# Kernel optimization log

Hardware: AMD Instinct MI355X
Metric: run time of the kernel (lower is better)

The kernel has to match this reference:

```python
import jax, jax.numpy as jnp
import numpy as np

TEMPERATURE_F = 0.5  # temperature_f from __init__


def setup_inputs() -> dict:
    key = jax.random.key(0)
    k1, k2 = jax.random.split(key)
    B, D = 4096, 512
    h_i = jax.random.normal(k1, (B, D), dtype=jnp.float32)
    h_j = jax.random.normal(k2, (B, D), dtype=jnp.float32)
    return {"h_i": h_i, "h_j": h_j}


def reference(h_i, h_j) -> jnp.ndarray:
    # NT-Xent loss (forward_private). N = 2*batch_size.
    B = h_i.shape[0]
    N = 2 * B
    h = jnp.concatenate([h_i, h_j], axis=0)          # [N, D]
    sim = (h @ h.T) / TEMPERATURE_F                   # [N, N]

    # Positive pairs: sim[i, i+B] and sim[i+B, i]
    sim_i_j = jnp.diagonal(sim, offset=B)             # [B]
    sim_j_i = jnp.diagonal(sim, offset=-B)            # [B]
    pos = jnp.concatenate([sim_i_j, sim_j_i], axis=0)  # [N]

    # Original builds logits = [pos | negatives] where negatives are the row of
    # sim with the diagonal and the positive entry removed, and labels are 0.
    # Cross-entropy per row = -pos_i + logsumexp(pos_i, negatives_i)
    #                       = -pos_i + logsumexp over row i of sim excluding the
    #                         diagonal (the positive entry equals pos_i, so the
    #                         set of logsumexp'd values is identical).
    neg_inf = jnp.finfo(sim.dtype).min
    diag = jnp.eye(N, dtype=bool)
    sim_masked = jnp.where(diag, neg_inf, sim)        # exclude self-similarity
    lse = jax.nn.logsumexp(sim_masked, axis=1)        # [N]

    loss = jnp.sum(lse - pos) / N                     # CE sum reduction, / N
    return loss
```

## Files before the change

kernel.cpp:

```cpp
#include <hip/hip_runtime.h>
#include <hip/hip_bf16.h>
#include <float.h>

#define BN_ 4096
#define DD  512
#define NN  8192
#define SCALE 2.0f

typedef unsigned short u16;
typedef __attribute__((ext_vector_type(8))) short short8;
typedef __attribute__((ext_vector_type(4))) float floatx4;

struct alignas(8) U16x4 { u16 x, y, z, w; };

__device__ __forceinline__ u16 f2bf(float f) {
    union { float f; unsigned u; } c; c.f = f;
    unsigned u = c.u;
    unsigned r = (u + 0x7fffu + ((u >> 16) & 1u)) >> 16;
    return (u16)r;
}

__device__ __forceinline__ void async_copy16(const u16* g, u16* l) {
    __builtin_amdgcn_global_load_lds(
        (const __attribute__((address_space(1))) void*)g,
        (__attribute__((address_space(3))) void*)l, 16, 0, 0);
}

__global__ __launch_bounds__(256) void convert_pos_kernel(const float* __restrict__ hi,
                                                          const float* __restrict__ hj,
                                                          u16* __restrict__ H,
                                                          float* __restrict__ out) {
    __shared__ float red[4];
    int t = blockIdx.x * 256 + threadIdx.x;
    int e = t * 4;
    const int BD = BN_ * DD;
    float4 a = *(const float4*)(hi + e);
    float4 b = *(const float4*)(hj + e);
    U16x4 oa, ob;
    oa.x = f2bf(a.x); oa.y = f2bf(a.y); oa.z = f2bf(a.z); oa.w = f2bf(a.w);
    ob.x = f2bf(b.x); ob.y = f2bf(b.y); ob.z = f2bf(b.z); ob.w = f2bf(b.w);
    *(U16x4*)(H + e) = oa;
    *(U16x4*)(H + BD + e) = ob;
    float dot = a.x * b.x + a.y * b.y + a.z * b.z + a.w * b.w;
#pragma unroll
    for (int msk = 1; msk < 64; msk <<= 1) dot += __shfl_xor(dot, msk);
    int lane = threadIdx.x & 63, wid = threadIdx.x >> 6;
    if (lane == 0) red[wid] = dot;
    __syncthreads();
    if (threadIdx.x == 0) {
        float s = red[0] + red[1] + red[2] + red[3];
        atomicAdd(out, s * (-4.0f / (float)NN));
    }
}

__global__ __launch_bounds__(256, 3) void gram_kernel(const u16* __restrict__ H,
                                                      float* __restrict__ Mpart,
                                                      float* __restrict__ Spart) {
    __shared__ u16 As[128 * 64];
    __shared__ u16 Bs[128 * 64];
    __shared__ float Rm[2][128], Rs[2][128];
    __shared__ float Cm[2][128], Cs[2][128];

    const int tid  = threadIdx.x;
    const int lane = tid & 63;
    const int wid  = tid >> 6;
    const int quad = lane >> 4;
    const int ln15 = lane & 15;
    const int wr = wid >> 1, wc = wid & 1;

    int t = blockIdx.x;
    int bi = (int)((sqrtf(8.0f * (float)t + 1.0f) - 1.0f) * 0.5f);
    while ((bi + 1) * (bi + 2) / 2 <= t) bi++;
    while (bi * (bi + 1) / 2 > t) bi--;
    const int bj = t - bi * (bi + 1) / 2;
    const bool diag = (bi == bj);
    const int biBase = bi * 128, bjBase = bj * 128;

    const u16* srcA[4];
    int ldsOff[4];
#pragma unroll
    for (int j = 0; j < 4; j++) {
        int c   = j * 256 + tid;
        int row = c >> 3;
        int kc  = (c & 7) ^ (row & 7);
        srcA[j]   = H + (size_t)(biBase + row) * DD + kc * 8;
        ldsOff[j] = c * 8;
    }
    const ptrdiff_t dB = (ptrdiff_t)(bjBase - biBase) * DD;

    floatx4 acc[4][4];
#pragma unroll
    for (int i = 0; i < 4; i++)
#pragma unroll
        for (int j = 0; j < 4; j++) acc[i][j] = (floatx4)0.0f;

    for (int k0 = 0; k0 < DD; k0 += 64) {
#pragma unroll
        for (int j = 0; j < 4; j++) async_copy16(srcA[j] + k0,      &As[ldsOff[j]]);
#pragma unroll
        for (int j = 0; j < 4; j++) async_copy16(srcA[j] + dB + k0, &Bs[ldsOff[j]]);
        __syncthreads();

#pragma unroll
        for (int kk = 0; kk < 2; kk++) {
            int ck = kk * 4 + quad;
            short8 a[4], b[4];
#pragma unroll
            for (int tm = 0; tm < 4; tm++) {
                int r = wr * 64 + tm * 16 + ln15;
                a[tm] = *(const short8*)&As[(r * 8 + (ck ^ (r & 7))) * 8];
            }
#pragma unroll
            for (int tn = 0; tn < 4; tn++) {
                int r = wc * 64 + tn * 16 + ln15;
                b[tn] = *(const short8*)&Bs[(r * 8 + (ck ^ (r & 7))) * 8];
            }
#pragma unroll
            for (int tm = 0; tm < 4; tm++)
#pragma unroll
                for (int tn = 0; tn < 4; tn++)
                    acc[tm][tn] = __builtin_amdgcn_mfma_f32_16x16x32_bf16(
                        a[tm], b[tn], acc[tm][tn], 0, 0, 0);
        }
        __syncthreads();
    }

#pragma unroll
    for (int tm = 0; tm < 4; tm++)
#pragma unroll
        for (int tn = 0; tn < 4; tn++)
#pragma unroll
            for (int r = 0; r < 4; r++) {
                float v = SCALE * acc[tm][tn][r];
                if (diag) {
                    int lrow = wr * 64 + tm * 16 + quad * 4 + r;
                    int lcol = wc * 64 + tn * 16 + ln15;
                    if (lrow == lcol) v = -FLT_MAX;
                }
                acc[tm][tn][r] = v;
            }

#pragma unroll
    for (int tm = 0; tm < 4; tm++) {
#pragma unroll
        for (int r = 0; r < 4; r++) {
            float vmax = -FLT_MAX;
#pragma unroll
            for (int tn = 0; tn < 4; tn++) vmax = fmaxf(vmax, acc[tm][tn][r]);
#pragma unroll
            for (int msk = 1; msk < 16; msk <<= 1)
                vmax = fmaxf(vmax, __shfl_xor(vmax, msk));
            float s = 0.0f;
#pragma unroll
            for (int tn = 0; tn < 4; tn++) s += __expf(acc[tm][tn][r] - vmax);
#pragma unroll
            for (int msk = 1; msk < 16; msk <<= 1) s += __shfl_xor(s, msk);
            if (ln15 == 0) {
                int x = wr * 64 + tm * 16 + quad * 4 + r;
                Rm[wc][x] = vmax; Rs[wc][x] = s;
            }
        }
    }

    if (!diag) {
#pragma unroll
        for (int tn = 0; tn < 4; tn++) {
            float cm = -FLT_MAX;
#pragma unroll
            for (int tm = 0; tm < 4; tm++)
#pragma unroll
                for (int r = 0; r < 4; r++) cm = fmaxf(cm, acc[tm][tn][r]);
            cm = fmaxf(cm, __shfl_xor(cm, 16));
            cm = fmaxf(cm, __shfl_xor(cm, 32));
            float s = 0.0f;
#pragma unroll
            for (int tm = 0; tm < 4; tm++)
#pragma unroll
                for (int r = 0; r < 4; r++) s += __expf(acc[tm][tn][r] - cm);
            s += __shfl_xor(s, 16);
            s += __shfl_xor(s, 32);
            if (quad == 0) {
                int y = wc * 64 + tn * 16 + ln15;
                Cm[wr][y] = cm; Cs[wr][y] = s;
            }
        }
    }
    __syncthreads();

    if (tid < 128) {
        float m0 = Rm[0][tid], m1 = Rm[1][tid];
        float s0 = Rs[0][tid], s1 = Rs[1][tid];
        float m = fmaxf(m0, m1);
        float s = s0 * __expf(m0 - m) + s1 * __expf(m1 - m);
        Mpart[(size_t)bj * NN + biBase + tid] = m;
        Spart[(size_t)bj * NN + biBase + tid] = s;
    } else if (!diag) {
        int y = tid - 128;
        float m0 = Cm[0][y], m1 = Cm[1][y];
        float s0 = Cs[0][y], s1 = Cs[1][y];
        float m = fmaxf(m0, m1);
        float s = s0 * __expf(m0 - m) + s1 * __expf(m1 - m);
        Mpart[(size_t)bi * NN + bjBase + y] = m;
        Spart[(size_t)bi * NN + bjBase + y] = s;
    }
}

__global__ __launch_bounds__(256) void lse_kernel(const float* __restrict__ Mpart,
                                                  const float* __restrict__ Spart,
                                                  float* __restrict__ out) {
    __shared__ float red[256];
    int tid = threadIdx.x;
    int r = blockIdx.x * 256 + tid;
    float m = -FLT_MAX, s = 0.0f;
#pragma unroll 8
    for (int c = 0; c < 64; c++) {
        float mc = Mpart[(size_t)c * NN + r];
        float sc = Spart[(size_t)c * NN + r];
        float mn = fmaxf(m, mc);
        s = s * __expf(m - mn) + sc * __expf(mc - mn);
        m = mn;
    }
    float lse = m + logf(s);
    red[tid] = lse;
    __syncthreads();
    for (int st = 128; st > 0; st >>= 1) {
        if (tid < st) red[tid] += red[tid + st];
        __syncthreads();
    }
    if (tid == 0) atomicAdd(out, red[0] * (1.0f / (float)NN));
}

extern "C" void kernel_launch(void* const* d_in, const int* in_sizes, int n_in,
                              void* d_out, int out_size, void* d_ws, size_t ws_size,
                              hipStream_t stream) {
    const float* hi = (const float*)d_in[0];
    const float* hj = (const float*)d_in[1];
    float* out = (float*)d_out;

    u16*   H     = (u16*)d_ws;
    float* Mpart = (float*)((char*)d_ws + (size_t)8 * 1024 * 1024);
    float* Spart = (float*)((char*)d_ws + (size_t)10 * 1024 * 1024);

    hipMemsetAsync(d_out, 0, sizeof(float), stream);

    convert_pos_kernel<<<2048, 256, 0, stream>>>(hi, hj, H, out);

    gram_kernel<<<2080, 256, 0, stream>>>(H, Mpart, Spart);

    lse_kernel<<<32, 256, 0, stream>>>(Mpart, Spart, out);
}
```

Baseline: 158.1 us.

## Use two waves per 128x128 gram tile with 64x128 per-wave subtiles

The gram kernel drops from four waves to two per block, and each wave computes a 64x128 subtile with 32 MFMA accumulators instead of 64x64. Because each wave now spans the full column width, the row reduction finishes inside the wave and is written straight to global memory, removing the cross-wave row merge through LDS. The aim is more MFMA work per LDS fragment load and less reduction overhead. In exchange each wave holds twice as many accumulator registers, and fewer waves per block plus the launch bound of 2 may reduce latency hiding.

```diff
diff --git a/kernel.cpp b/kernel.cpp
--- a/kernel.cpp
+++ b/kernel.cpp
@@ -53,12 +53,11 @@
     }
 }
 
-__global__ __launch_bounds__(256, 3) void gram_kernel(const u16* __restrict__ H,
+__global__ __launch_bounds__(128, 2) void gram_kernel(const u16* __restrict__ H,
                                                       float* __restrict__ Mpart,
                                                       float* __restrict__ Spart) {
     __shared__ u16 As[128 * 64];
     __shared__ u16 Bs[128 * 64];
-    __shared__ float Rm[2][128], Rs[2][128];
     __shared__ float Cm[2][128], Cs[2][128];
 
     const int tid  = threadIdx.x;
@@ -66,7 +65,6 @@
     const int wid  = tid >> 6;
     const int quad = lane >> 4;
     const int ln15 = lane & 15;
-    const int wr = wid >> 1, wc = wid & 1;
 
     int t = blockIdx.x;
     int bi = (int)((sqrtf(8.0f * (float)t + 1.0f) - 1.0f) * 0.5f);
@@ -76,11 +74,11 @@
     const bool diag = (bi == bj);
     const int biBase = bi * 128, bjBase = bj * 128;
 
-    const u16* srcA[4];
-    int ldsOff[4];
-#pragma unroll
-    for (int j = 0; j < 4; j++) {
-        int c   = j * 256 + tid;
+    const u16* srcA[8];
+    int ldsOff[8];
+#pragma unroll
+    for (int j = 0; j < 8; j++) {
+        int c   = j * 128 + tid;
         int row = c >> 3;
         int kc  = (c & 7) ^ (row & 7);
         srcA[j]   = H + (size_t)(biBase + row) * DD + kc * 8;
@@ -88,37 +86,37 @@
     }
     const ptrdiff_t dB = (ptrdiff_t)(bjBase - biBase) * DD;
 
-    floatx4 acc[4][4];
+    floatx4 acc[4][8];
 #pragma unroll
     for (int i = 0; i < 4; i++)
 #pragma unroll
-        for (int j = 0; j < 4; j++) acc[i][j] = (floatx4)0.0f;
+        for (int j = 0; j < 8; j++) acc[i][j] = (floatx4)0.0f;
 
     for (int k0 = 0; k0 < DD; k0 += 64) {
 #pragma unroll
-        for (int j = 0; j < 4; j++) async_copy16(srcA[j] + k0,      &As[ldsOff[j]]);
-#pragma unroll
-        for (int j = 0; j < 4; j++) async_copy16(srcA[j] + dB + k0, &Bs[ldsOff[j]]);
+        for (int j = 0; j < 8; j++) async_copy16(srcA[j] + k0,      &As[ldsOff[j]]);
+#pragma unroll
+        for (int j = 0; j < 8; j++) async_copy16(srcA[j] + dB + k0, &Bs[ldsOff[j]]);
         __syncthreads();
 
 #pragma unroll
         for (int kk = 0; kk < 2; kk++) {
             int ck = kk * 4 + quad;
-            short8 a[4], b[4];
+            short8 a[4], b[8];
 #pragma unroll
             for (int tm = 0; tm < 4; tm++) {
-                int r = wr * 64 + tm * 16 + ln15;
+                int r = wid * 64 + tm * 16 + ln15;
                 a[tm] = *(const short8*)&As[(r * 8 + (ck ^ (r & 7))) * 8];
             }
 #pragma unroll
-            for (int tn = 0; tn < 4; tn++) {
-                int r = wc * 64 + tn * 16 + ln15;
+            for (int tn = 0; tn < 8; tn++) {
+                int r = tn * 16 + ln15;
                 b[tn] = *(const short8*)&Bs[(r * 8 + (ck ^ (r & 7))) * 8];
             }
 #pragma unroll
             for (int tm = 0; tm < 4; tm++)
 #pragma unroll
-                for (int tn = 0; tn < 4; tn++)
+                for (int tn = 0; tn < 8; tn++)
                     acc[tm][tn] = __builtin_amdgcn_mfma_f32_16x16x32_bf16(
                         a[tm], b[tn], acc[tm][tn], 0, 0, 0);
         }
@@ -128,13 +126,13 @@
 #pragma unroll
     for (int tm = 0; tm < 4; tm++)
 #pragma unroll
-        for (int tn = 0; tn < 4; tn++)
+        for (int tn = 0; tn < 8; tn++)
 #pragma unroll
             for (int r = 0; r < 4; r++) {
                 float v = SCALE * acc[tm][tn][r];
                 if (diag) {
-                    int lrow = wr * 64 + tm * 16 + quad * 4 + r;
-                    int lcol = wc * 64 + tn * 16 + ln15;
+                    int lrow = wid * 64 + tm * 16 + quad * 4 + r;
+                    int lcol = tn * 16 + ln15;
                     if (lrow == lcol) v = -FLT_MAX;
                 }
                 acc[tm][tn][r] = v;
@@ -146,25 +144,26 @@
         for (int r = 0; r < 4; r++) {
             float vmax = -FLT_MAX;
 #pragma unroll
-            for (int tn = 0; tn < 4; tn++) vmax = fmaxf(vmax, acc[tm][tn][r]);
+            for (int tn = 0; tn < 8; tn++) vmax = fmaxf(vmax, acc[tm][tn][r]);
 #pragma unroll
             for (int msk = 1; msk < 16; msk <<= 1)
                 vmax = fmaxf(vmax, __shfl_xor(vmax, msk));
             float s = 0.0f;
 #pragma unroll
-            for (int tn = 0; tn < 4; tn++) s += __expf(acc[tm][tn][r] - vmax);
+            for (int tn = 0; tn < 8; tn++) s += __expf(acc[tm][tn][r] - vmax);
 #pragma unroll
             for (int msk = 1; msk < 16; msk <<= 1) s += __shfl_xor(s, msk);
             if (ln15 == 0) {
-                int x = wr * 64 + tm * 16 + quad * 4 + r;
-                Rm[wc][x] = vmax; Rs[wc][x] = s;
+                int grow = biBase + wid * 64 + tm * 16 + quad * 4 + r;
+                Mpart[(size_t)bj * NN + grow] = vmax;
+                Spart[(size_t)bj * NN + grow] = s;
             }
         }
     }
 
     if (!diag) {
 #pragma unroll
-        for (int tn = 0; tn < 4; tn++) {
+        for (int tn = 0; tn < 8; tn++) {
             float cm = -FLT_MAX;
 #pragma unroll
             for (int tm = 0; tm < 4; tm++)
@@ -180,28 +179,20 @@
             s += __shfl_xor(s, 16);
             s += __shfl_xor(s, 32);
             if (quad == 0) {
-                int y = wc * 64 + tn * 16 + ln15;
-                Cm[wr][y] = cm; Cs[wr][y] = s;
+                int y = tn * 16 + ln15;
+                Cm[wid][y] = cm; Cs[wid][y] = s;
             }
         }
     }
     __syncthreads();
 
-    if (tid < 128) {
-        float m0 = Rm[0][tid], m1 = Rm[1][tid];
-        float s0 = Rs[0][tid], s1 = Rs[1][tid];
+    if (!diag) {
+        float m0 = Cm[0][tid], m1 = Cm[1][tid];
+        float s0 = Cs[0][tid], s1 = Cs[1][tid];
         float m = fmaxf(m0, m1);
         float s = s0 * __expf(m0 - m) + s1 * __expf(m1 - m);
-        Mpart[(size_t)bj * NN + biBase + tid] = m;
-        Spart[(size_t)bj * NN + biBase + tid] = s;
-    } else if (!diag) {
-        int y = tid - 128;
-        float m0 = Cm[0][y], m1 = Cm[1][y];
-        float s0 = Cs[0][y], s1 = Cs[1][y];
-        float m = fmaxf(m0, m1);
-        float s = s0 * __expf(m0 - m) + s1 * __expf(m1 - m);
-        Mpart[(size_t)bi * NN + bjBase + y] = m;
-        Spart[(size_t)bi * NN + bjBase + y] = s;
+        Mpart[(size_t)bi * NN + bjBase + tid] = m;
+        Spart[(size_t)bi * NN + bjBase + tid] = s;
     }
 }
 
@@ -245,7 +236,7 @@
 
     convert_pos_kernel<<<2048, 256, 0, stream>>>(hi, hj, H, out);
 
-    gram_kernel<<<2080, 256, 0, stream>>>(H, Mpart, Spart);
+    gram_kernel<<<2080, 128, 0, stream>>>(H, Mpart, Spart);
 
     lse_kernel<<<32, 256, 0, stream>>>(Mpart, Spart, out);
 }
```

New measurement: 162.1 us. 1.03x slower.
